# Performance work log

Measured on AMD Instinct MI355X. Metric: run time of the kernel, lower is better.

## Reference

```python
import jax, jax.numpy as jnp
import numpy as np

THRESH = 0.5  # original code thresholds raw span logit channel 0 at 0.5


def setup_inputs() -> dict:
    key = jax.random.key(0)
    ks = jax.random.split(key, 9)
    B, S, H, P = 4, 256, 768, 54  # P = num_spo_patterns + 1
    scale = 0.02
    return {
        "sequence_output": jax.random.normal(ks[0], (B, S, H), jnp.float32),
        "W1s": jax.random.normal(ks[1], (H, H), jnp.float32) * scale,
        "b1s": jnp.zeros((H,), jnp.float32),
        "W2s": jax.random.normal(ks[2], (2, H), jnp.float32) * scale,
        "b2s": jnp.zeros((2,), jnp.float32),
        "Wp1": jax.random.normal(ks[3], (H, 2 * H), jnp.float32) * scale,
        "bp1": jnp.zeros((H,), jnp.float32),
        "Wp2": jax.random.normal(ks[4], (P, H), jnp.float32) * scale,
        "bp2": jnp.zeros((P,), jnp.float32),
    }


def reference(sequence_output, W1s, b1s, W2s, b2s, Wp1, bp1, Wp2, bp2):
    x = sequence_output                                # [B,S,H]
    B, S, H = x.shape
    # span classifier: Linear -> ReLU -> Linear
    h = jax.nn.relu(jnp.einsum('bsh,kh->bsk', x, W1s) + b1s)
    span_logits = jnp.einsum('bsh,kh->bsk', h, W2s) + b2s   # [B,S,2]
    cand = span_logits[..., 0] > THRESH                      # [B,S] candidates
    # spo pattern classifier on concat pairs: Linear(2H,H) splits into two H->H maps
    Wa, Wb = Wp1[:, :H], Wp1[:, H:]                          # subject / object halves
    ha = jnp.einsum('bsh,kh->bsk', x, Wa)                    # [B,S,H]
    hb = jnp.einsum('bsh,kh->bsk', x, Wb)                    # [B,S,H]
    pair_hidden = jax.nn.relu(ha[:, :, None, :] + hb[:, None, :, :] + bp1)  # [B,S,S,H]
    pair_logits = jnp.einsum('bijh,ph->bijp', pair_hidden, Wp2) + bp2       # [B,S,S,P]
    # valid pairs: both are candidates and subj != obj (diagonal excluded)
    not_diag = ~jnp.eye(S, dtype=bool)
    valid = cand[:, :, None] & cand[:, None, :] & not_diag   # [B,S,S]
    # dense masked equivalent of the per-pair Python loop (invalid pairs zeroed,
    # matching the zeros fallback for empty candidate sets)
    spo_pattern_logits = jnp.where(valid[..., None], pair_logits, 0.0)
    return spo_pattern_logits
```

## Files before the change

### kernel.cpp

```cpp
#include <hip/hip_runtime.h>
#include <hip/hip_bf16.h>


#define M_ROWS 1024
#define HDIM 768
#define PDIM 54
#define MAXC 256
#define KCHUNK 16
#define NKC (HDIM / KCHUNK)
#define KSPLIT 4
#define KSEG (HDIM / KSPLIT)

#define CANDCNT_OFF  0
#define PAIRCNT_OFF  4
#define CANDIDX_OFF  8192
#define CANDSLOT_OFF 12288
#define PAIR_OFF     16384
#define HPART_OFF    1064960

__global__ __launch_bounds__(256) void gemm_k_kernel(
    const float* __restrict__ x, const float* __restrict__ W1,
    float* __restrict__ hpart, int* __restrict__ counters)
{
    __shared__ float As[16][68];
    __shared__ float Bs[16][68];

    if (blockIdx.x == 0 && blockIdx.y == 0 && blockIdx.z == 0 && threadIdx.x < 2)
        counters[threadIdx.x] = 0;

    const int m0 = blockIdx.x * 64;
    const int n0 = blockIdx.y * 64;
    const int kb = blockIdx.z * KSEG;
    const int t  = threadIdx.x;
    const int tm = t & 15;
    const int tn = t >> 4;
    const int r  = t >> 2;
    const int c4 = (t & 3) * 4;

    float acc[4][4] = {};

    for (int k0 = kb; k0 < kb + KSEG; k0 += 16) {
        float4 av = *(const float4*)(x  + (size_t)(m0 + r) * HDIM + k0 + c4);
        float4 bv = *(const float4*)(W1 + (size_t)(n0 + r) * HDIM + k0 + c4);
        As[c4+0][r] = av.x; As[c4+1][r] = av.y; As[c4+2][r] = av.z; As[c4+3][r] = av.w;
        Bs[c4+0][r] = bv.x; Bs[c4+1][r] = bv.y; Bs[c4+2][r] = bv.z; Bs[c4+3][r] = bv.w;
        __syncthreads();
        #pragma unroll
        for (int kk = 0; kk < 16; ++kk) {
            float a[4], b[4];
            #pragma unroll
            for (int i = 0; i < 4; ++i) a[i] = As[kk][tm * 4 + i];
            #pragma unroll
            for (int j = 0; j < 4; ++j) b[j] = Bs[kk][tn * 4 + j];
            #pragma unroll
            for (int i = 0; i < 4; ++i)
                #pragma unroll
                for (int j = 0; j < 4; ++j)
                    acc[i][j] += a[i] * b[j];
        }
        __syncthreads();
    }

    float* dst = hpart + (size_t)blockIdx.z * (M_ROWS * HDIM);
    #pragma unroll
    for (int i = 0; i < 4; ++i) {
        float4 v = make_float4(acc[i][0], acc[i][1], acc[i][2], acc[i][3]);
        *(float4*)(dst + (size_t)(m0 + tm * 4 + i) * HDIM + n0 + tn * 4) = v;
    }
}

__global__ __launch_bounds__(256) void span_cand_kernel(
    const float* __restrict__ hpart, const float* __restrict__ b1,
    const float* __restrict__ w2row, const float* __restrict__ b2,
    int* __restrict__ candCount, int* __restrict__ candIdx,
    int* __restrict__ candSlot)
{
    const int m = blockIdx.x;
    const int t = threadIdx.x;
    float p = 0.f;
    for (int n = t; n < HDIM; n += 256) {
        float v = hpart[(size_t)m * HDIM + n]
                + hpart[(size_t)(M_ROWS * HDIM) + (size_t)m * HDIM + n]
                + hpart[(size_t)(2 * M_ROWS * HDIM) + (size_t)m * HDIM + n]
                + hpart[(size_t)(3 * M_ROWS * HDIM) + (size_t)m * HDIM + n];
        v += b1[n];
        v = v > 0.f ? v : 0.f;
        p += v * w2row[n];
    }
    __shared__ float wred[4];
    #pragma unroll
    for (int off = 32; off > 0; off >>= 1) p += __shfl_down(p, off, 64);
    if ((t & 63) == 0) wred[t >> 6] = p;
    __syncthreads();
    if (t == 0) {
        float s = wred[0] + wred[1] + wred[2] + wred[3] + b2[0];
        if (s > 0.5f) {
            int sl = atomicAdd(candCount, 1);
            if (sl < MAXC) { candIdx[sl] = m; candSlot[m] = sl; }
            else candSlot[m] = -1;
        } else {
            candSlot[m] = -1;
        }
    }
}

__global__ __launch_bounds__(256) void hab_kernel(
    const float* __restrict__ x, const float* __restrict__ Wp1,
    const int* __restrict__ candCount, const int* __restrict__ candIdx,
    float* __restrict__ ha, float* __restrict__ hb)
{
    __shared__ float xs[HDIM];
    __shared__ float red[2][KCHUNK][17];
    int nc = *candCount; if (nc > MAXC) nc = MAXC;
    const int nitems = nc * NKC;
    const int kk  = threadIdx.x >> 4;
    const int hb0 = (threadIdx.x & 15) * 4;

    for (int item = blockIdx.x; item < nitems; item += gridDim.x) {
        int slot = item / NKC;
        int kc   = item % NKC;
        int row  = candIdx[slot];

        for (int h = threadIdx.x; h < HDIM; h += 256)
            xs[h] = x[(size_t)row * HDIM + h];
        __syncthreads();

        int k = kc * KCHUNK + kk;
        const float* wr = Wp1 + (size_t)k * (2 * HDIM);
        float sa = 0.f, sb = 0.f;
        #pragma unroll
        for (int h = hb0; h < HDIM; h += 64) {
            float4 xv = *(const float4*)(xs + h);
            float4 wa = *(const float4*)(wr + h);
            float4 wb = *(const float4*)(wr + HDIM + h);
            sa += xv.x * wa.x + xv.y * wa.y + xv.z * wa.z + xv.w * wa.w;
            sb += xv.x * wb.x + xv.y * wb.y + xv.z * wb.z + xv.w * wb.w;
        }
        red[0][kk][threadIdx.x & 15] = sa;
        red[1][kk][threadIdx.x & 15] = sb;
        __syncthreads();

        if (threadIdx.x < 32) {
            int which = threadIdx.x >> 4;
            int kk2   = threadIdx.x & 15;
            float s = 0.f;
            #pragma unroll
            for (int g = 0; g < 16; ++g) s += red[which][kk2][g];
            float* dst = which == 0 ? ha : hb;
            dst[(size_t)slot * HDIM + kc * KCHUNK + kk2] = s;
        }
        __syncthreads();
    }
}

__global__ void pairs_kernel(const int* __restrict__ candSlot,
                             int* __restrict__ pairCount, int* __restrict__ pairList)
{
    int idx = blockIdx.x * 256 + threadIdx.x;
    int b = idx >> 16;
    int i = (idx >> 8) & 255;
    int j = idx & 255;
    if (i == j) return;
    if (candSlot[b * 256 + i] >= 0 && candSlot[b * 256 + j] >= 0) {
        int p = atomicAdd(pairCount, 1);
        pairList[p] = idx;
    }
}

__global__ __launch_bounds__(256) void pair_kernel(
    const float* __restrict__ ha, const float* __restrict__ hb,
    const float* __restrict__ bp1, const float* __restrict__ Wp2,
    const float* __restrict__ bp2, const int* __restrict__ candSlot,
    const int* __restrict__ pairCount, const int* __restrict__ pairList,
    float* __restrict__ out)
{
    __shared__ float v[HDIM];
    __shared__ float red[4][PDIM + 2];
    const int np = *pairCount;
    const int t = threadIdx.x;
    for (int p = blockIdx.x; p < np; p += gridDim.x) {
        int idx = pairList[p];
        int b = idx >> 16;
        int i = (idx >> 8) & 255;
        int j = idx & 255;
        int si = candSlot[b * 256 + i];
        int sj = candSlot[b * 256 + j];
        if (t < 192) {
            float4 a4 = *(const float4*)(ha + (size_t)si * HDIM + t * 4);
            float4 b4 = *(const float4*)(hb + (size_t)sj * HDIM + t * 4);
            float4 c4 = *(const float4*)(bp1 + t * 4);
            float4 r;
            r.x = a4.x + b4.x + c4.x; r.x = r.x > 0.f ? r.x : 0.f;
            r.y = a4.y + b4.y + c4.y; r.y = r.y > 0.f ? r.y : 0.f;
            r.z = a4.z + b4.z + c4.z; r.z = r.z > 0.f ? r.z : 0.f;
            r.w = a4.w + b4.w + c4.w; r.w = r.w > 0.f ? r.w : 0.f;
            *(float4*)(v + t * 4) = r;
        }
        __syncthreads();
        if (t < 216) {
            int pp  = t % PDIM;
            int seg = t / PDIM;
            const float* w = Wp2 + (size_t)pp * HDIM + seg * 192;
            const float* vv = v + seg * 192;
            float s = 0.f;
            for (int h = 0; h < 192; h += 4) {
                float4 a = *(const float4*)(vv + h);
                float4 b2_ = *(const float4*)(w + h);
                s += a.x * b2_.x + a.y * b2_.y + a.z * b2_.z + a.w * b2_.w;
            }
            red[seg][pp] = s;
        }
        __syncthreads();
        if (t < PDIM)
            out[(size_t)idx * PDIM + t] = red[0][t] + red[1][t] + red[2][t] + red[3][t] + bp2[t];
        __syncthreads();
    }
}

extern "C" void kernel_launch(void* const* d_in, const int* in_sizes, int n_in,
                              void* d_out, int out_size, void* d_ws, size_t ws_size,
                              hipStream_t stream) {
    const float* x   = (const float*)d_in[0];
    const float* W1s = (const float*)d_in[1];
    const float* b1s = (const float*)d_in[2];
    const float* W2s = (const float*)d_in[3];
    const float* b2s = (const float*)d_in[4];
    const float* Wp1 = (const float*)d_in[5];
    const float* bp1 = (const float*)d_in[6];
    const float* Wp2 = (const float*)d_in[7];
    const float* bp2 = (const float*)d_in[8];

    char* ws = (char*)d_ws;
    int*   counters = (int*)(ws + CANDCNT_OFF);
    int*   candCnt  = counters;
    int*   pairCnt  = counters + 1;
    int*   candIdx  = (int*)(ws + CANDIDX_OFF);
    int*   candSlot = (int*)(ws + CANDSLOT_OFF);
    int*   pairList = (int*)(ws + PAIR_OFF);
    float* hpart    = (float*)(ws + HPART_OFF);
    float* ha       = hpart + (size_t)KSPLIT * M_ROWS * HDIM;
    float* hb       = ha + (size_t)MAXC * HDIM;
    float* out = (float*)d_out;

    hipMemsetAsync(out, 0, (size_t)out_size * sizeof(float), stream);

    dim3 g(M_ROWS / 64, HDIM / 64, KSPLIT);
    gemm_k_kernel<<<g, 256, 0, stream>>>(x, W1s, hpart, counters);

    span_cand_kernel<<<M_ROWS, 256, 0, stream>>>(hpart, b1s, W2s, b2s,
                                                 candCnt, candIdx, candSlot);

    hab_kernel<<<2048, 256, 0, stream>>>(x, Wp1, candCnt, candIdx, ha, hb);

    pairs_kernel<<<1024, 256, 0, stream>>>(candSlot, pairCnt, pairList);

    pair_kernel<<<512, 256, 0, stream>>>(ha, hb, bp1, Wp2, bp2,
                                         candSlot, pairCnt, pairList, out);
}
```

Before: 139.3 us.

## Enlarge span GEMM tiles, fuse pair listing and output zeroing into hab kernel

The span GEMM moves to 128x128 tiles with an 8x8 per-thread register tile and an 8-way K split, so more work is done per block and per shared-memory load. The pair-listing kernel and the output memset are folded into the hab kernel as an extra set of blocks, which removes two launches and lets those jobs run alongside the hab projection. The risks are higher register pressure in the GEMM, fewer GEMM blocks (384), and twice as much partial-sum traffic for span_cand to reduce.

```diff
diff --git a/kernel.cpp b/kernel.cpp
--- a/kernel.cpp
+++ b/kernel.cpp
@@ -8,8 +8,11 @@
 #define MAXC 256
 #define KCHUNK 16
 #define NKC (HDIM / KCHUNK)
-#define KSPLIT 4
+#define KSPLIT 8
 #define KSEG (HDIM / KSPLIT)
+
+#define PAIRGRID 1024
+#define HABGRID  2048
 
 #define CANDCNT_OFF  0
 #define PAIRCNT_OFF  4
@@ -22,14 +25,14 @@
     const float* __restrict__ x, const float* __restrict__ W1,
     float* __restrict__ hpart, int* __restrict__ counters)
 {
-    __shared__ float As[16][68];
-    __shared__ float Bs[16][68];
+    __shared__ float As[16][132];
+    __shared__ float Bs[16][132];
 
     if (blockIdx.x == 0 && blockIdx.y == 0 && blockIdx.z == 0 && threadIdx.x < 2)
         counters[threadIdx.x] = 0;
 
-    const int m0 = blockIdx.x * 64;
-    const int n0 = blockIdx.y * 64;
+    const int m0 = blockIdx.x * 128;
+    const int n0 = blockIdx.y * 128;
     const int kb = blockIdx.z * KSEG;
     const int t  = threadIdx.x;
     const int tm = t & 15;
@@ -37,25 +40,33 @@
     const int r  = t >> 2;
     const int c4 = (t & 3) * 4;
 
-    float acc[4][4] = {};
+    float acc[8][8] = {};
 
     for (int k0 = kb; k0 < kb + KSEG; k0 += 16) {
-        float4 av = *(const float4*)(x  + (size_t)(m0 + r) * HDIM + k0 + c4);
-        float4 bv = *(const float4*)(W1 + (size_t)(n0 + r) * HDIM + k0 + c4);
-        As[c4+0][r] = av.x; As[c4+1][r] = av.y; As[c4+2][r] = av.z; As[c4+3][r] = av.w;
-        Bs[c4+0][r] = bv.x; Bs[c4+1][r] = bv.y; Bs[c4+2][r] = bv.z; Bs[c4+3][r] = bv.w;
+        #pragma unroll
+        for (int rr = 0; rr < 128; rr += 64) {
+            float4 av = *(const float4*)(x  + (size_t)(m0 + rr + r) * HDIM + k0 + c4);
+            float4 bv = *(const float4*)(W1 + (size_t)(n0 + rr + r) * HDIM + k0 + c4);
+            As[c4+0][rr+r] = av.x; As[c4+1][rr+r] = av.y;
+            As[c4+2][rr+r] = av.z; As[c4+3][rr+r] = av.w;
+            Bs[c4+0][rr+r] = bv.x; Bs[c4+1][rr+r] = bv.y;
+            Bs[c4+2][rr+r] = bv.z; Bs[c4+3][rr+r] = bv.w;
+        }
         __syncthreads();
         #pragma unroll
         for (int kk = 0; kk < 16; ++kk) {
-            float a[4], b[4];
+            float a[8], b[8];
             #pragma unroll
-            for (int i = 0; i < 4; ++i) a[i] = As[kk][tm * 4 + i];
+            for (int i = 0; i < 4; ++i) {
+                a[i]     = As[kk][tm * 4 + i];
+                a[i + 4] = As[kk][64 + tm * 4 + i];
+                b[i]     = Bs[kk][tn * 4 + i];
+                b[i + 4] = Bs[kk][64 + tn * 4 + i];
+            }
             #pragma unroll
-            for (int j = 0; j < 4; ++j) b[j] = Bs[kk][tn * 4 + j];
-            #pragma unroll
-            for (int i = 0; i < 4; ++i)
+            for (int i = 0; i < 8; ++i)
                 #pragma unroll
-                for (int j = 0; j < 4; ++j)
+                for (int j = 0; j < 8; ++j)
                     acc[i][j] += a[i] * b[j];
         }
         __syncthreads();
@@ -63,9 +74,14 @@
 
     float* dst = hpart + (size_t)blockIdx.z * (M_ROWS * HDIM);
     #pragma unroll
-    for (int i = 0; i < 4; ++i) {
-        float4 v = make_float4(acc[i][0], acc[i][1], acc[i][2], acc[i][3]);
-        *(float4*)(dst + (size_t)(m0 + tm * 4 + i) * HDIM + n0 + tn * 4) = v;
+    for (int ii = 0; ii < 8; ++ii) {
+        int row = m0 + (ii >> 2) * 64 + tm * 4 + (ii & 3);
+        #pragma unroll
+        for (int h = 0; h < 2; ++h) {
+            float4 v = make_float4(acc[ii][h*4+0], acc[ii][h*4+1],
+                                   acc[ii][h*4+2], acc[ii][h*4+3]);
+            *(float4*)(dst + (size_t)row * HDIM + n0 + h * 64 + tn * 4) = v;
+        }
     }
 }
 
@@ -79,10 +95,10 @@
     const int t = threadIdx.x;
     float p = 0.f;
     for (int n = t; n < HDIM; n += 256) {
-        float v = hpart[(size_t)m * HDIM + n]
-                + hpart[(size_t)(M_ROWS * HDIM) + (size_t)m * HDIM + n]
-                + hpart[(size_t)(2 * M_ROWS * HDIM) + (size_t)m * HDIM + n]
-                + hpart[(size_t)(3 * M_ROWS * HDIM) + (size_t)m * HDIM + n];
+        float v = 0.f;
+        #pragma unroll
+        for (int z = 0; z < KSPLIT; ++z)
+            v += hpart[(size_t)z * (M_ROWS * HDIM) + (size_t)m * HDIM + n];
         v += b1[n];
         v = v > 0.f ? v : 0.f;
         p += v * w2row[n];
@@ -104,11 +120,31 @@
     }
 }
 
-__global__ __launch_bounds__(256) void hab_kernel(
+__global__ __launch_bounds__(256) void hab_pairs_kernel(
     const float* __restrict__ x, const float* __restrict__ Wp1,
     const int* __restrict__ candCount, const int* __restrict__ candIdx,
-    float* __restrict__ ha, float* __restrict__ hb)
-{
+    float* __restrict__ ha, float* __restrict__ hb,
+    const int* __restrict__ candSlot,
+    int* __restrict__ pairCount, int* __restrict__ pairList,
+    float* __restrict__ out)
+{
+    if (blockIdx.x < PAIRGRID) {
+        const int pb = blockIdx.x;
+        float4* dst = (float4*)(out + (size_t)pb * 256 * PDIM);
+        const float4 z4 = make_float4(0.f, 0.f, 0.f, 0.f);
+        for (int f = threadIdx.x; f < 256 * PDIM / 4; f += 256)
+            dst[f] = z4;
+        int idx = pb * 256 + threadIdx.x;
+        int b = idx >> 16;
+        int i = (idx >> 8) & 255;
+        int j = idx & 255;
+        if (i != j && candSlot[b * 256 + i] >= 0 && candSlot[b * 256 + j] >= 0) {
+            int p = atomicAdd(pairCount, 1);
+            pairList[p] = idx;
+        }
+        return;
+    }
+
     __shared__ float xs[HDIM];
     __shared__ float red[2][KCHUNK][17];
     int nc = *candCount; if (nc > MAXC) nc = MAXC;
@@ -116,7 +152,7 @@
     const int kk  = threadIdx.x >> 4;
     const int hb0 = (threadIdx.x & 15) * 4;
 
-    for (int item = blockIdx.x; item < nitems; item += gridDim.x) {
+    for (int item = blockIdx.x - PAIRGRID; item < nitems; item += HABGRID) {
         int slot = item / NKC;
         int kc   = item % NKC;
         int row  = candIdx[slot];
@@ -146,24 +182,10 @@
             float s = 0.f;
             #pragma unroll
             for (int g = 0; g < 16; ++g) s += red[which][kk2][g];
-            float* dst = which == 0 ? ha : hb;
-            dst[(size_t)slot * HDIM + kc * KCHUNK + kk2] = s;
-        }
-        __syncthreads();
-    }
-}
-
-__global__ void pairs_kernel(const int* __restrict__ candSlot,
-                             int* __restrict__ pairCount, int* __restrict__ pairList)
-{
-    int idx = blockIdx.x * 256 + threadIdx.x;
-    int b = idx >> 16;
-    int i = (idx >> 8) & 255;
-    int j = idx & 255;
-    if (i == j) return;
-    if (candSlot[b * 256 + i] >= 0 && candSlot[b * 256 + j] >= 0) {
-        int p = atomicAdd(pairCount, 1);
-        pairList[p] = idx;
+            float* dstp = which == 0 ? ha : hb;
+            dstp[(size_t)slot * HDIM + kc * KCHUNK + kk2] = s;
+        }
+        __syncthreads();
     }
 }
 
@@ -242,17 +264,14 @@
     float* hb       = ha + (size_t)MAXC * HDIM;
     float* out = (float*)d_out;
 
-    hipMemsetAsync(out, 0, (size_t)out_size * sizeof(float), stream);
-
-    dim3 g(M_ROWS / 64, HDIM / 64, KSPLIT);
+    dim3 g(M_ROWS / 128, HDIM / 128, KSPLIT);
     gemm_k_kernel<<<g, 256, 0, stream>>>(x, W1s, hpart, counters);
 
     span_cand_kernel<<<M_ROWS, 256, 0, stream>>>(hpart, b1s, W2s, b2s,
                                                  candCnt, candIdx, candSlot);
 
-    hab_kernel<<<2048, 256, 0, stream>>>(x, Wp1, candCnt, candIdx, ha, hb);
-
-    pairs_kernel<<<1024, 256, 0, stream>>>(candSlot, pairCnt, pairList);
+    hab_pairs_kernel<<<PAIRGRID + HABGRID, 256, 0, stream>>>(
+        x, Wp1, candCnt, candIdx, ha, hb, candSlot, pairCnt, pairList, out);
 
     pair_kernel<<<512, 256, 0, stream>>>(ha, hb, bp1, Wp2, bp2,
                                          candSlot, pairCnt, pairList, out);
```

New measurement: 140.9 us. About the same (+1.2%).
